# Kernel optimization log

Hardware: AMD Instinct MI355X
Metric: run time of the kernel (lower is better)

## Reference

```python
import jax, jax.numpy as jnp
import numpy as np


def a_powers(A, t):
    # A: [K, n, n]; returns [t, K, n, n] = stack(I, A, A^2, ..., A^(t-1))
    K, n, _ = A.shape
    result = jnp.broadcast_to(jnp.eye(n, dtype=A.dtype), (1, K, n, n))
    lift = A
    while result.shape[0] < t:
        result = jnp.concatenate([result, result @ lift], axis=0)
        lift = lift @ lift
    return result[:t]


def fast_conv_real(a, b):
    # a: [len1, K, n, n], b: [batch, len2, K, n] -> conv(b, a): [batch, len1+len2-1, K, n]
    len1 = a.shape[0]
    len2 = b.shape[1]
    T = 2 ** int(np.ceil(np.log2(len1 + len2 - 1)))
    Af = jnp.fft.rfft(a, n=T, axis=0)
    Bf = jnp.fft.rfft(b, n=T, axis=1)
    Cf = jnp.einsum('blki,lkij->blkj', Bf, Af)
    c = jnp.fft.irfft(Cf, n=T, axis=1)
    return c[:, :len1 + len2 - 1]


def setup_inputs() -> dict:
    key = jax.random.key(0)
    k_u, k_x0, k_theta, k_B, k_C = jax.random.split(key, 5)
    batch, length = 8, 4096
    input_size, state_size, output_size = 256, 256, 256
    blk = 2
    K = state_size // blk  # 128
    u = jax.random.normal(k_u, (batch, length, input_size), dtype=jnp.float32)
    x0 = jax.random.normal(k_x0, (batch, K, blk), dtype=jnp.float32)
    # A initialized as K random 2x2 rotation blocks (as in __init__)
    theta = 2 * jnp.pi * jax.random.uniform(k_theta, (K,), dtype=jnp.float32)
    c, s = jnp.cos(theta), jnp.sin(theta)
    A = jnp.stack([jnp.stack([c, s], -1), jnp.stack([-s, c], -1)], -2)  # [K, 2, 2]
    B = jax.random.normal(k_B, (input_size, state_size), dtype=jnp.float32) / (state_size + input_size) ** 0.5
    C = jax.random.normal(k_C, (state_size, output_size), dtype=jnp.float32) / (state_size + output_size) ** 0.5
    return {"u": u, "x0": x0, "A": A, "B": B, "C": C}


def reference(u, x0, A, B, C):
    batch, length, _ = u.shape
    K, blk, _ = A.shape
    Aps = a_powers(A, length + 1)          # [length+1, K, blk, blk]
    uB = (u @ B).reshape(batch, length, K, blk)
    x = fast_conv_real(Aps[:-1], uB)[:, :length]  # [batch, length, K, blk]
    x = x + jnp.einsum('bki,lkij->blkj', x0, Aps[1:])
    new_state = x[:, -1]                    # [batch, K, blk]
    y = x.reshape(batch, length, K * blk) @ C
    return (y, new_state)
```

## Files before the change

### kernel.cpp

```cpp
#include <hip/hip_runtime.h>
#include <hip/hip_bf16.h>

typedef __bf16 bf16x2_t __attribute__((ext_vector_type(2)));
typedef __bf16 bf16x8_t __attribute__((ext_vector_type(8)));
typedef float f32x4 __attribute__((ext_vector_type(4)));

#define BATCH   8
#define LENGTH  4096
#define KHALF   128
#define MTOT    (BATCH*LENGTH)
#define NCHUNK  128
#define LC      32

#define SWZ(ch, row) ((ch) ^ ((row) & 7))

__global__ __launch_bounds__(256) void transpose_bc(
    const float* __restrict__ Bsrc, const float* __restrict__ Csrc,
    __bf16* __restrict__ BT, __bf16* __restrict__ CT) {
  const float* src = blockIdx.y ? Csrc : Bsrc;
  __bf16* dst      = blockIdx.y ? CT   : BT;
  int n  = blockIdx.x;
  int kk = threadIdx.x;
  dst[n * 256 + kk] = (__bf16)src[kk * 256 + n];
}

__global__ __launch_bounds__(256) void gemm1_fused(
    const float* __restrict__ u, const __bf16* __restrict__ BT,
    const float* __restrict__ Aarr,
    __bf16* __restrict__ uB, float2* __restrict__ P) {
  __shared__ __align__(16) __bf16 sA[64 * 256];

  const int tid  = threadIdx.x;
  const int lane = tid & 63;
  const int wave = tid >> 6;
  const int m_l  = lane & 15, quad = lane >> 4;
  const int m0   = blockIdx.x * 64;
  const int b    = m0 >> 12;
  const int t0   = m0 & 4095;

#pragma unroll
  for (int i = 0; i < 8; ++i) {
    int s   = tid + i * 256;
    int row = s >> 5, ch = s & 31;
    const float4* g = (const float4*)(u + (size_t)(m0 + row) * 256 + ch * 8);
    float4 a = g[0], c = g[1];
    bf16x8_t v;
    v[0]=(__bf16)a.x; v[1]=(__bf16)a.y; v[2]=(__bf16)a.z; v[3]=(__bf16)a.w;
    v[4]=(__bf16)c.x; v[5]=(__bf16)c.y; v[6]=(__bf16)c.z; v[7]=(__bf16)c.w;
    *(bf16x8_t*)&sA[row * 256 + SWZ(ch, row) * 8] = v;
  }
  __syncthreads();

  f32x4 acc[4][4];
#pragma unroll
  for (int mi = 0; mi < 4; ++mi)
#pragma unroll
    for (int ni = 0; ni < 4; ++ni)
#pragma unroll
      for (int r = 0; r < 4; ++r) acc[mi][ni][r] = 0.f;

#pragma unroll
  for (int kc8 = 0; kc8 < 8; ++kc8) {
    bf16x8_t af[4], bfr[4];
#pragma unroll
    for (int mi = 0; mi < 4; ++mi) {
      int row = mi * 16 + m_l;
      int c   = kc8 * 4 + quad;
      af[mi] = *(const bf16x8_t*)&sA[row * 256 + SWZ(c, row) * 8];
    }
#pragma unroll
    for (int ni = 0; ni < 4; ++ni) {
      int n = wave * 64 + ni * 16 + m_l;
      bfr[ni] = *(const bf16x8_t*)(BT + (size_t)n * 256 + kc8 * 32 + quad * 8);
    }
#pragma unroll
    for (int mi = 0; mi < 4; ++mi)
#pragma unroll
      for (int ni = 0; ni < 4; ++ni)
        acc[mi][ni] = __builtin_amdgcn_mfma_f32_16x16x32_bf16(af[mi], bfr[ni], acc[mi][ni], 0, 0, 0);
  }
  __syncthreads();

  __bf16* sT = sA;
#pragma unroll
  for (int mi = 0; mi < 4; ++mi)
#pragma unroll
    for (int ni = 0; ni < 4; ++ni)
#pragma unroll
      for (int r = 0; r < 4; ++r) {
        int row = mi * 16 + quad * 4 + r;
        int col = wave * 64 + ni * 16 + m_l;
        sT[row * 256 + SWZ(col >> 3, row) * 8 + (col & 7)] = (__bf16)acc[mi][ni][r];
      }
  __syncthreads();

#pragma unroll
  for (int i = 0; i < 8; ++i) {
    int s   = tid + i * 256;
    int row = s >> 5, ch = s & 31;
    *(bf16x8_t*)(uB + (size_t)(m0 + row) * 256 + ch * 8) =
        *(const bf16x8_t*)&sT[row * 256 + SWZ(ch, row) * 8];
  }

  {
    int k   = tid & 127;
    int chl = tid >> 7;
    float cc = Aarr[4 * k], sv = Aarr[4 * k + 1];
    float hr = 0.f, hi = 0.f;
#pragma unroll 8
    for (int j = 0; j < LC; ++j) {
      int row = chl * 32 + j;
      bf16x2_t v2 = *(const bf16x2_t*)&sT[row * 256 + SWZ(k >> 2, row) * 8 + ((2 * k) & 7)];
      float t = fmaf(hr, cc, fmaf(-hi, sv, (float)v2[0]));
      hi      = fmaf(hr, sv, fmaf( hi, cc, (float)v2[1]));
      hr = t;
    }
    int chg = (t0 >> 5) + chl;
    P[((size_t)b * NCHUNK + chg) * KHALF + k] = make_float2(hr, hi);
  }
}

__global__ __launch_bounds__(256) void gemm2_fused(
    const __bf16* __restrict__ uB, const float* __restrict__ Aarr,
    const float* __restrict__ x0, const float2* __restrict__ P,
    const __bf16* __restrict__ CT,
    float* __restrict__ state_out, float* __restrict__ Y) {
  __shared__ __align__(16) __bf16 sX[64 * 256];

  const int tid  = threadIdx.x;
  const int lane = tid & 63;
  const int wave = tid >> 6;
  const int m_l  = lane & 15, quad = lane >> 4;
  const int m0   = blockIdx.x * 64;
  const int b    = m0 >> 12;
  const int t0   = m0 & 4095;

#pragma unroll
  for (int i = 0; i < 8; ++i) {
    int s   = tid + i * 256;
    int row = s >> 5, ch = s & 31;
    *(bf16x8_t*)&sX[row * 256 + SWZ(ch, row) * 8] =
        *(const bf16x8_t*)(uB + (size_t)(m0 + row) * 256 + ch * 8);
  }

  const int k   = tid & 127;
  const int chl = tid >> 7;
  const int chg = (t0 >> 5) + chl;
  const float cc = Aarr[4 * k], sv = Aarr[4 * k + 1];
  float carry_r, carry_i;
  {
    float wr = cc, wi = sv;
#pragma unroll
    for (int i = 0; i < 5; ++i) { float nr = wr*wr - wi*wi; wi = 2.f*wr*wi; wr = nr; }
    float hr = x0[b * 256 + 2 * k], hi = x0[b * 256 + 2 * k + 1];
    const float2* pp = P + (size_t)b * NCHUNK * KHALF + k;
#pragma unroll 4
    for (int ch = 0; ch < chg; ++ch) {
      float2 pv = pp[(size_t)ch * KHALF];
      float t = fmaf(hr, wr, fmaf(-hi, wi, pv.x));
      hi      = fmaf(hr, wi, fmaf( hi, wr, pv.y));
      hr = t;
    }
    carry_r = hr; carry_i = hi;
  }
  __syncthreads();

  {
    float hr = carry_r, hi = carry_i;
#pragma unroll 8
    for (int j = 0; j < LC; ++j) {
      int row = chl * 32 + j;
      int idx = row * 256 + SWZ(k >> 2, row) * 8 + ((2 * k) & 7);
      bf16x2_t v2 = *(const bf16x2_t*)&sX[idx];
      float t = fmaf(hr, cc, fmaf(-hi, sv, (float)v2[0]));
      hi      = fmaf(hr, sv, fmaf( hi, cc, (float)v2[1]));
      hr = t;
      bf16x2_t o; o[0] = (__bf16)hr; o[1] = (__bf16)hi;
      *(bf16x2_t*)&sX[idx] = o;
    }
    if (t0 == 4032 && chl == 1) {
      state_out[b * 256 + 2 * k]     = hr;
      state_out[b * 256 + 2 * k + 1] = hi;
    }
  }
  __syncthreads();

  f32x4 acc[4][4];
#pragma unroll
  for (int mi = 0; mi < 4; ++mi)
#pragma unroll
    for (int ni = 0; ni < 4; ++ni)
#pragma unroll
      for (int r = 0; r < 4; ++r) acc[mi][ni][r] = 0.f;

#pragma unroll
  for (int kc8 = 0; kc8 < 8; ++kc8) {
    bf16x8_t af[4], bfr[4];
#pragma unroll
    for (int mi = 0; mi < 4; ++mi) {
      int row = mi * 16 + m_l;
      int c   = kc8 * 4 + quad;
      af[mi] = *(const bf16x8_t*)&sX[row * 256 + SWZ(c, row) * 8];
    }
#pragma unroll
    for (int ni = 0; ni < 4; ++ni) {
      int n = wave * 64 + ni * 16 + m_l;
      bfr[ni] = *(const bf16x8_t*)(CT + (size_t)n * 256 + kc8 * 32 + quad * 8);
    }
#pragma unroll
    for (int mi = 0; mi < 4; ++mi)
#pragma unroll
      for (int ni = 0; ni < 4; ++ni)
        acc[mi][ni] = __builtin_amdgcn_mfma_f32_16x16x32_bf16(af[mi], bfr[ni], acc[mi][ni], 0, 0, 0);
  }

#pragma unroll
  for (int mi = 0; mi < 4; ++mi)
#pragma unroll
    for (int ni = 0; ni < 4; ++ni)
#pragma unroll
      for (int r = 0; r < 4; ++r) {
        int row = m0 + mi * 16 + quad * 4 + r;
        int col = wave * 64 + ni * 16 + m_l;
        Y[(size_t)row * 256 + col] = acc[mi][ni][r];
      }
}

extern "C" void kernel_launch(void* const* d_in, const int* in_sizes, int n_in,
                              void* d_out, int out_size, void* d_ws, size_t ws_size,
                              hipStream_t stream) {
  const float* u  = (const float*)d_in[0];
  const float* x0 = (const float*)d_in[1];
  const float* A  = (const float*)d_in[2];
  const float* B  = (const float*)d_in[3];
  const float* C  = (const float*)d_in[4];

  float* y         = (float*)d_out;
  float* state_out = y + (size_t)MTOT * 256;

  char* ws = (char*)d_ws;
  __bf16* BT = (__bf16*)ws;  ws += 256 * 256 * 2;
  __bf16* CT = (__bf16*)ws;  ws += 256 * 256 * 2;
  __bf16* uB = (__bf16*)ws;  ws += (size_t)MTOT * 256 * 2;
  float2* P  = (float2*)ws;  ws += (size_t)BATCH * NCHUNK * KHALF * sizeof(float2);

  transpose_bc<<<dim3(256, 2), 256, 0, stream>>>(B, C, BT, CT);
  gemm1_fused<<<dim3(MTOT / 64), 256, 0, stream>>>(u, BT, A, uB, P);
  gemm2_fused<<<dim3(MTOT / 64), 256, 0, stream>>>(uB, A, x0, P, CT, state_out, y);
}
```

Baseline: 124.4 us.

## Fuse both GEMM passes into one persistent kernel with a grid-wide atomic barrier

Merges the two fused GEMM kernels into a single kernel. Each block keeps its projected u@B tile in shared memory across an atomic-counter grid barrier, then runs the carry propagation and the C GEMM. This removes the round trip of the bf16 uB intermediate through global memory and one kernel launch. In exchange it adds a spin-wait barrier and a memset of the counter. It relies on all 512 blocks being co-resident at two blocks per CU; if they are not, the kernel deadlocks.

```diff
diff --git a/kernel.cpp b/kernel.cpp
--- a/kernel.cpp
+++ b/kernel.cpp
@@ -11,6 +11,7 @@
 #define MTOT    (BATCH*LENGTH)
 #define NCHUNK  128
 #define LC      32
+#define NBLK    (MTOT/64)
 
 #define SWZ(ch, row) ((ch) ^ ((row) & 7))
 
@@ -24,11 +25,13 @@
   dst[n * 256 + kk] = (__bf16)src[kk * 256 + n];
 }
 
-__global__ __launch_bounds__(256) void gemm1_fused(
+__global__ __launch_bounds__(256, 2) void ssm_persistent(
     const float* __restrict__ u, const __bf16* __restrict__ BT,
-    const float* __restrict__ Aarr,
-    __bf16* __restrict__ uB, float2* __restrict__ P) {
-  __shared__ __align__(16) __bf16 sA[64 * 256];
+    const __bf16* __restrict__ CT, const float* __restrict__ Aarr,
+    const float* __restrict__ x0,
+    float2* __restrict__ P, unsigned* __restrict__ cnt,
+    float* __restrict__ state_out, float* __restrict__ Y) {
+  __shared__ __align__(16) __bf16 sT[64 * 256];
 
   const int tid  = threadIdx.x;
   const int lane = tid & 63;
@@ -47,7 +50,7 @@
     bf16x8_t v;
     v[0]=(__bf16)a.x; v[1]=(__bf16)a.y; v[2]=(__bf16)a.z; v[3]=(__bf16)a.w;
     v[4]=(__bf16)c.x; v[5]=(__bf16)c.y; v[6]=(__bf16)c.z; v[7]=(__bf16)c.w;
-    *(bf16x8_t*)&sA[row * 256 + SWZ(ch, row) * 8] = v;
+    *(bf16x8_t*)&sT[row * 256 + SWZ(ch, row) * 8] = v;
   }
   __syncthreads();
 
@@ -66,7 +69,7 @@
     for (int mi = 0; mi < 4; ++mi) {
       int row = mi * 16 + m_l;
       int c   = kc8 * 4 + quad;
-      af[mi] = *(const bf16x8_t*)&sA[row * 256 + SWZ(c, row) * 8];
+      af[mi] = *(const bf16x8_t*)&sT[row * 256 + SWZ(c, row) * 8];
     }
 #pragma unroll
     for (int ni = 0; ni < 4; ++ni) {
@@ -81,7 +84,6 @@
   }
   __syncthreads();
 
-  __bf16* sT = sA;
 #pragma unroll
   for (int mi = 0; mi < 4; ++mi)
 #pragma unroll
@@ -94,18 +96,11 @@
       }
   __syncthreads();
 
-#pragma unroll
-  for (int i = 0; i < 8; ++i) {
-    int s   = tid + i * 256;
-    int row = s >> 5, ch = s & 31;
-    *(bf16x8_t*)(uB + (size_t)(m0 + row) * 256 + ch * 8) =
-        *(const bf16x8_t*)&sT[row * 256 + SWZ(ch, row) * 8];
-  }
-
+  const int k   = tid & 127;
+  const int chl = tid >> 7;
+  const int chg = (t0 >> 5) + chl;
+  const float cc = Aarr[4 * k], sv = Aarr[4 * k + 1];
   {
-    int k   = tid & 127;
-    int chl = tid >> 7;
-    float cc = Aarr[4 * k], sv = Aarr[4 * k + 1];
     float hr = 0.f, hi = 0.f;
 #pragma unroll 8
     for (int j = 0; j < LC; ++j) {
@@ -115,38 +110,18 @@
       hi      = fmaf(hr, sv, fmaf( hi, cc, (float)v2[1]));
       hr = t;
     }
-    int chg = (t0 >> 5) + chl;
     P[((size_t)b * NCHUNK + chg) * KHALF + k] = make_float2(hr, hi);
   }
-}
-
-__global__ __launch_bounds__(256) void gemm2_fused(
-    const __bf16* __restrict__ uB, const float* __restrict__ Aarr,
-    const float* __restrict__ x0, const float2* __restrict__ P,
-    const __bf16* __restrict__ CT,
-    float* __restrict__ state_out, float* __restrict__ Y) {
-  __shared__ __align__(16) __bf16 sX[64 * 256];
-
-  const int tid  = threadIdx.x;
-  const int lane = tid & 63;
-  const int wave = tid >> 6;
-  const int m_l  = lane & 15, quad = lane >> 4;
-  const int m0   = blockIdx.x * 64;
-  const int b    = m0 >> 12;
-  const int t0   = m0 & 4095;
-
-#pragma unroll
-  for (int i = 0; i < 8; ++i) {
-    int s   = tid + i * 256;
-    int row = s >> 5, ch = s & 31;
-    *(bf16x8_t*)&sX[row * 256 + SWZ(ch, row) * 8] =
-        *(const bf16x8_t*)(uB + (size_t)(m0 + row) * 256 + ch * 8);
-  }
-
-  const int k   = tid & 127;
-  const int chl = tid >> 7;
-  const int chg = (t0 >> 5) + chl;
-  const float cc = Aarr[4 * k], sv = Aarr[4 * k + 1];
+
+  __syncthreads();
+  __threadfence();
+  if (tid == 0) {
+    atomicAdd(cnt, 1u);
+    while (__hip_atomic_load(cnt, __ATOMIC_ACQUIRE, __HIP_MEMORY_SCOPE_AGENT) < NBLK)
+      __builtin_amdgcn_s_sleep(2);
+  }
+  __syncthreads();
+
   float carry_r, carry_i;
   {
     float wr = cc, wi = sv;
@@ -163,7 +138,6 @@
     }
     carry_r = hr; carry_i = hi;
   }
-  __syncthreads();
 
   {
     float hr = carry_r, hi = carry_i;
@@ -171,12 +145,12 @@
     for (int j = 0; j < LC; ++j) {
       int row = chl * 32 + j;
       int idx = row * 256 + SWZ(k >> 2, row) * 8 + ((2 * k) & 7);
-      bf16x2_t v2 = *(const bf16x2_t*)&sX[idx];
+      bf16x2_t v2 = *(const bf16x2_t*)&sT[idx];
       float t = fmaf(hr, cc, fmaf(-hi, sv, (float)v2[0]));
       hi      = fmaf(hr, sv, fmaf( hi, cc, (float)v2[1]));
       hr = t;
       bf16x2_t o; o[0] = (__bf16)hr; o[1] = (__bf16)hi;
-      *(bf16x2_t*)&sX[idx] = o;
+      *(bf16x2_t*)&sT[idx] = o;
     }
     if (t0 == 4032 && chl == 1) {
       state_out[b * 256 + 2 * k]     = hr;
@@ -185,7 +159,6 @@
   }
   __syncthreads();
 
-  f32x4 acc[4][4];
 #pragma unroll
   for (int mi = 0; mi < 4; ++mi)
 #pragma unroll
@@ -200,7 +173,7 @@
     for (int mi = 0; mi < 4; ++mi) {
       int row = mi * 16 + m_l;
       int c   = kc8 * 4 + quad;
-      af[mi] = *(const bf16x8_t*)&sX[row * 256 + SWZ(c, row) * 8];
+      af[mi] = *(const bf16x8_t*)&sT[row * 256 + SWZ(c, row) * 8];
     }
 #pragma unroll
     for (int ni = 0; ni < 4; ++ni) {
@@ -239,12 +212,12 @@
   float* state_out = y + (size_t)MTOT * 256;
 
   char* ws = (char*)d_ws;
-  __bf16* BT = (__bf16*)ws;  ws += 256 * 256 * 2;
-  __bf16* CT = (__bf16*)ws;  ws += 256 * 256 * 2;
-  __bf16* uB = (__bf16*)ws;  ws += (size_t)MTOT * 256 * 2;
-  float2* P  = (float2*)ws;  ws += (size_t)BATCH * NCHUNK * KHALF * sizeof(float2);
-
+  __bf16* BT   = (__bf16*)ws;    ws += 256 * 256 * 2;
+  __bf16* CT   = (__bf16*)ws;    ws += 256 * 256 * 2;
+  float2* P    = (float2*)ws;    ws += (size_t)BATCH * NCHUNK * KHALF * sizeof(float2);
+  unsigned* cnt = (unsigned*)ws; ws += 256;
+
+  hipMemsetAsync(cnt, 0, 256, stream);
   transpose_bc<<<dim3(256, 2), 256, 0, stream>>>(B, C, BT, CT);
-  gemm1_fused<<<dim3(MTOT / 64), 256, 0, stream>>>(u, BT, A, uB, P);
-  gemm2_fused<<<dim3(MTOT / 64), 256, 0, stream>>>(uB, A, x0, P, CT, state_out, y);
+  ssm_persistent<<<dim3(NBLK), 256, 0, stream>>>(u, BT, CT, A, x0, P, cnt, state_out, y);
 }
```

After: 182.6 us. 46.8% more time.
